# Kernel tuning notes

Hardware: AMD Instinct MI355X
Metric: run time of the kernel (lower is better)

The kernel has to match this reference:

```python
import jax, jax.numpy as jnp
import numpy as np

B, P, M, N, H = 2, 2048, 1024, 16, 64
NEG = 1e10


def setup_inputs() -> dict:
    key = jax.random.key(0)
    ks = jax.random.split(key, 8)
    std = 0.02
    return {
        "x": jax.random.normal(ks[0], (B, P, M), jnp.float32),
        "kernel_query": std * jax.random.normal(ks[1], (N, M, H), jnp.float32),
        "bias_query": jnp.zeros((N, H), jnp.float32),
        "kernel_key": std * jax.random.normal(ks[2], (N, M, H), jnp.float32),
        "bias_key": jnp.zeros((N, H), jnp.float32),
        "kernel_value": std * jax.random.normal(ks[3], (N, M, H), jnp.float32),
        "bias_value": jnp.zeros((N, H), jnp.float32),
        "kernel_out": std * jax.random.normal(ks[4], (N, H, M), jnp.float32),
        "bias_out": jnp.zeros((M,), jnp.float32),
    }


def reference(x, kernel_query, bias_query, kernel_key, bias_key,
              kernel_value, bias_value, kernel_out, bias_out):
    # per-head projections: [b,p,m] x [n,m,h] -> [b,p,n,h]
    q = jnp.einsum('bpm,nmh->bpnh', x, kernel_query) + bias_query
    k = jnp.einsum('bpm,nmh->bpnh', x, kernel_key) + bias_key
    v = jnp.einsum('bpm,nmh->bpnh', x, kernel_value) + bias_value

    # explicit score matrix [b,n,pq,pk]
    scores = jnp.einsum('bqnh,bknh->bnqk', q, k) / jnp.sqrt(jnp.float32(H))
    # faithful reproduction of original (inverted) mask: keep strictly-upper
    # triangle, subtract 1e10 elsewhere
    p = scores.shape[-1]
    mask = jnp.triu(jnp.ones((p, p), scores.dtype), k=1)  # [pq,pk]
    masked = scores * mask - NEG * (1.0 - mask)
    attn = jax.nn.softmax(masked, axis=-1)

    z = jnp.einsum('bknh,bnqk->bqnh', v, attn)
    return jnp.einsum('bqnh,nhm->bqm', z, kernel_out) + bias_out
```

## Files before the change

kernel.cpp:

```cpp
#include <hip/hip_runtime.h>

typedef __attribute__((ext_vector_type(8))) __bf16 bf16x8;
typedef __attribute__((ext_vector_type(4))) float  f32x4;
typedef unsigned short u16;
typedef unsigned int   u32;

__device__ __forceinline__ u16 f2b(float f) {
  u32 u = __builtin_bit_cast(u32, f);
  u32 r = (u + 0x7FFFu + ((u >> 16) & 1u)) >> 16;
  return (u16)r;
}

typedef __attribute__((address_space(3))) void lds_void;
typedef const __attribute__((address_space(1))) void gbl_void;

__device__ __forceinline__ void gload_lds16(const u16* g, u16* l) {
  __builtin_amdgcn_global_load_lds((gbl_void*)g, (lds_void*)l, 16, 0, 0);
}

#define QSCALE 0.18033688011112042f
#define MFIX   4.328085122666891f

__global__ __launch_bounds__(256) void prep_all(const float* __restrict__ x,
                                                const float* __restrict__ wq,
                                                const float* __restrict__ wk,
                                                const float* __restrict__ wv,
                                                const float* __restrict__ wo,
                                                u16* __restrict__ xb,
                                                u16* __restrict__ wbt,
                                                u16* __restrict__ wot) {
  int bid = blockIdx.x;
  int tid = threadIdx.x;
  if (bid < 4096) {
    int i = bid * 256 + tid;
    float4 v = ((const float4*)x)[i];
    ushort4 o;
    o.x = f2b(v.x); o.y = f2b(v.y); o.z = f2b(v.z); o.w = f2b(v.w);
    ((ushort4*)xb)[i] = o;
    return;
  }
  __shared__ float t[64][65];
  int sub = bid - 4096;
  const float* src; u16* dst; int sstride, dstride, r0, c0;
  if (sub < 768) {
    int proj = sub >> 8, rem = sub & 255;
    int ym = rem >> 4, xt = rem & 15;
    src = ((proj == 0) ? wq : (proj == 1) ? wk : wv) + (size_t)ym * 65536;
    dst = wbt + ((size_t)proj << 20) + (size_t)ym * 65536;
    sstride = 64; dstride = 1024; r0 = xt * 64; c0 = 0;
  } else {
    int s2 = sub - 768;
    src = wo; dst = wot;
    sstride = 1024; dstride = 1024;
    r0 = (s2 & 15) * 64; c0 = (s2 >> 4) * 64;
  }
  int rr = tid >> 2, q = tid & 3;
#pragma unroll
  for (int i = 0; i < 4; ++i) {
    float4 v = *(const float4*)&src[(size_t)(r0 + rr) * sstride + c0 + q * 16 + i * 4];
    t[rr][q * 16 + i * 4 + 0] = v.x;
    t[rr][q * 16 + i * 4 + 1] = v.y;
    t[rr][q * 16 + i * 4 + 2] = v.z;
    t[rr][q * 16 + i * 4 + 3] = v.w;
  }
  __syncthreads();
  int cc = rr;
#pragma unroll
  for (int i = 0; i < 4; ++i) {
    ushort4 o;
    o.x = f2b(t[q * 16 + i * 4 + 0][cc]);
    o.y = f2b(t[q * 16 + i * 4 + 1][cc]);
    o.z = f2b(t[q * 16 + i * 4 + 2][cc]);
    o.w = f2b(t[q * 16 + i * 4 + 3][cc]);
    *(ushort4*)&dst[(size_t)(c0 + cc) * dstride + r0 + q * 16 + i * 4] = o;
  }
}

__global__ __launch_bounds__(256) void gemm_qkv(const u16* __restrict__ xb,
                                                const u16* __restrict__ wbt,
                                                const float* __restrict__ bq,
                                                const float* __restrict__ bk,
                                                const float* __restrict__ bv,
                                                u16* __restrict__ qb,
                                                u16* __restrict__ kbf,
                                                u16* __restrict__ vtb) {
  __shared__ __align__(16) u16 As[128 * 32];
  __shared__ __align__(16) u16 Bs[64 * 32];
  f32x4 acc[4][2];
#pragma unroll
  for (int mi = 0; mi < 4; ++mi)
#pragma unroll
    for (int ni = 0; ni < 2; ++ni) acc[mi][ni] = (f32x4){0.f, 0.f, 0.f, 0.f};

  int bid = blockIdx.x;
  int rt = bid & 31, ct = bid >> 5;
  int R0 = rt * 128, C0 = ct * 64;

  int tid = threadIdx.x;
  int w = tid >> 6, l = tid & 63;
  int lr = l & 15, lg = l >> 4;
  int wr = w >> 1, wc = w & 1;

  for (int k0 = 0; k0 < 1024; k0 += 32) {
#pragma unroll
    for (int i = 0; i < 2; ++i) {
      int t = w * 2 + i;
      gload_lds16(xb + (size_t)(R0 + t * 16 + (l >> 2)) * 1024 + k0 + (l & 3) * 8, &As[t * 512]);
    }
    gload_lds16(wbt + (size_t)(C0 + w * 16 + (l >> 2)) * 1024 + k0 + (l & 3) * 8, &Bs[w * 512]);
    __syncthreads();
    bf16x8 af[4], bfr[2];
#pragma unroll
    for (int mi = 0; mi < 4; ++mi)
      af[mi] = *(const bf16x8*)&As[(wr * 64 + mi * 16 + lr) * 32 + lg * 8];
#pragma unroll
    for (int ni = 0; ni < 2; ++ni)
      bfr[ni] = *(const bf16x8*)&Bs[(wc * 32 + ni * 16 + lr) * 32 + lg * 8];
#pragma unroll
    for (int mi = 0; mi < 4; ++mi)
#pragma unroll
      for (int ni = 0; ni < 2; ++ni)
        acc[mi][ni] = __builtin_amdgcn_mfma_f32_16x16x32_bf16(af[mi], bfr[ni], acc[mi][ni], 0, 0, 0);
    __syncthreads();
  }

  int proj = C0 >> 10;
#pragma unroll
  for (int ni = 0; ni < 2; ++ni) {
    int col = C0 + wc * 32 + ni * 16 + lr;
    int within = col & 1023;
    int n = within >> 6, h = within & 63;
    const float* bias = (proj == 0) ? bq : (proj == 1 ? bk : bv);
    float badd = bias[within];
    float scl = (proj == 0) ? QSCALE : 1.0f;
#pragma unroll
    for (int mi = 0; mi < 4; ++mi) {
#pragma unroll
      for (int r = 0; r < 4; ++r) {
        int row = R0 + wr * 64 + mi * 16 + lg * 4 + r;
        int b = row >> 11, p = row & 2047;
        int bn = b * 16 + n;
        u16 u = f2b((acc[mi][ni][r] + badd) * scl);
        if (proj == 0)      qb [((size_t)bn * 2048 + p) * 64 + h] = u;
        else if (proj == 1) kbf[((size_t)bn * 2048 + p) * 64 + h] = u;
        else                vtb[(((size_t)bn * 32 + (p >> 6)) * 64 + h) * 64 + (p & 63)] = u;
      }
    }
  }
}

__global__ __launch_bounds__(256) void mean_v(const u16* __restrict__ vtb,
                                              u16* __restrict__ zb) {
  __shared__ float red[4][64];
  int bn = blockIdx.x;
  int w = threadIdx.x >> 6, h = threadIdx.x & 63;
  const u16* base = vtb + (size_t)bn * 131072 + (size_t)h * 64;
  float acc = 0.f;
  for (int pb = w; pb < 32; pb += 4) {
    const u16* r = base + (size_t)pb * 4096;
#pragma unroll
    for (int c = 0; c < 8; ++c) {
      bf16x8 v = *(const bf16x8*)(r + c * 8);
#pragma unroll
      for (int j = 0; j < 8; ++j) acc += (float)v[j];
    }
  }
  red[w][h] = acc;
  __syncthreads();
  if (w == 0) {
    float s = (red[0][h] + red[1][h] + red[2][h] + red[3][h]) * (1.0f / 2048.0f);
    int b = bn >> 4, n = bn & 15;
    zb[((size_t)(b * 2048 + 2047) * 16 + n) * 64 + h] = f2b(s);
  }
}

#define ATTN_STEP(BUFC, MASKED)                                                \
  {                                                                            \
    if (t + 1 < trips) {                                                       \
      gload_lds16(sk,       &Ks[BUFC ^ 1][w * 1024]);                          \
      gload_lds16(sk + 512, &Ks[BUFC ^ 1][w * 1024 + 512]);                    \
      gload_lds16(sv,       &Vs[BUFC ^ 1][w * 1024]);                          \
      gload_lds16(sv + 512, &Vs[BUFC ^ 1][w * 1024 + 512]);                    \
      sk += 4096; sv += 4096;                                                  \
      asm volatile("s_waitcnt vmcnt(4)" ::: "memory");                         \
    } else {                                                                   \
      asm volatile("s_waitcnt vmcnt(0)" ::: "memory");                         \
    }                                                                          \
    __builtin_amdgcn_s_barrier();                                              \
    asm volatile("" ::: "memory");                                             \
    f32x4 sacc[4];                                                             \
    __builtin_amdgcn_s_setprio(1);                                             \
    _Pragma("unroll") for (int nb = 0; nb < 4; ++nb) {                         \
      int row = nb * 16 + lr, sw = row & 7;                                    \
      bf16x8 kf0 = *(const bf16x8*)&Ks[BUFC][row * 64 + ((lg ^ sw) << 3)];     \
      bf16x8 kf1 = *(const bf16x8*)&Ks[BUFC][row * 64 + (((lg + 4) ^ sw) << 3)]; \
      f32x4 s = (f32x4){0.f, 0.f, 0.f, 0.f};                                   \
      s = __builtin_amdgcn_mfma_f32_16x16x32_bf16(qf0, kf0, s, 0, 0, 0);       \
      s = __builtin_amdgcn_mfma_f32_16x16x32_bf16(qf1, kf1, s, 0, 0, 0);       \
      sacc[nb] = s;                                                            \
    }                                                                          \
    __builtin_amdgcn_s_setprio(0);                                             \
    u16 pbv[4][4];                                                             \
    if (MASKED) {                                                              \
      _Pragma("unroll") for (int nb = 0; nb < 4; ++nb) {                       \
        int key = nb * 16 + lr;                                                \
        _Pragma("unroll") for (int r = 0; r < 4; ++r) {                        \
          int qrow = w * 16 + lg * 4 + r;                                      \
          float xv = (key > qrow) ? sacc[nb][r] : -1.0e10f;                    \
          float pe = __builtin_amdgcn_exp2f(xv - MFIX);                        \
          rsum[r] += pe;                                                       \
          pbv[nb][r] = __builtin_bit_cast(u16, (__bf16)pe);                    \
        }                                                                      \
      }                                                                        \
    } else {                                                                   \
      _Pragma("unroll") for (int nb = 0; nb < 4; ++nb)                         \
        _Pragma("unroll") for (int r = 0; r < 4; ++r) {                        \
          float pe = __builtin_amdgcn_exp2f(sacc[nb][r] - MFIX);               \
          rsum[r] += pe;                                                       \
          pbv[nb][r] = __builtin_bit_cast(u16, (__bf16)pe);                    \
        }                                                                      \
    }                                                                          \
    _Pragma("unroll") for (int nb = 0; nb < 4; ++nb)                           \
      _Pragma("unroll") for (int r = 0; r < 4; ++r) {                          \
        int prow = lg * 4 + r;                                                 \
        Plds[w][prow * 64 + ((((nb * 2) + (lr >> 3)) ^ (prow & 7)) << 3) + (lr & 7)] = pbv[nb][r]; \
      }                                                                        \
    asm volatile("s_waitcnt lgkmcnt(0)" ::: "memory");                         \
    __builtin_amdgcn_sched_barrier(0);                                         \
    bf16x8 pf0 = *(const bf16x8*)&Plds[w][lr * 64 + ((lg ^ (lr & 7)) << 3)];   \
    bf16x8 pf1 = *(const bf16x8*)&Plds[w][lr * 64 + (((4 + lg) ^ (lr & 7)) << 3)]; \
    __builtin_amdgcn_s_setprio(1);                                             \
    _Pragma("unroll") for (int hb = 0; hb < 4; ++hb) {                         \
      int row = hb * 16 + lr, sw = row & 7;                                    \
      bf16x8 vf0 = *(const bf16x8*)&Vs[BUFC][row * 64 + ((lg ^ sw) << 3)];     \
      bf16x8 vf1 = *(const bf16x8*)&Vs[BUFC][row * 64 + (((lg + 4) ^ sw) << 3)]; \
      oacc[hb] = __builtin_amdgcn_mfma_f32_16x16x32_bf16(pf0, vf0, oacc[hb], 0, 0, 0); \
      oacc[hb] = __builtin_amdgcn_mfma_f32_16x16x32_bf16(pf1, vf1, oacc[hb], 0, 0, 0); \
    }                                                                          \
    __builtin_amdgcn_s_setprio(0);                                             \
    asm volatile("" ::: "memory");                                             \
    __builtin_amdgcn_s_barrier();                                              \
    ++t;                                                                       \
  }

__global__ __launch_bounds__(256, 4) void attn_kern(const u16* __restrict__ qb,
                                                    const u16* __restrict__ kbf,
                                                    const u16* __restrict__ vtb,
                                                    u16* __restrict__ zb) {
  __shared__ __align__(16) u16 Ks[2][4096];
  __shared__ __align__(16) u16 Vs[2][4096];
  __shared__ __align__(16) u16 Plds[4][1024];

  int bid = blockIdx.x;
  int bn = bid & 31, c = bid >> 5;
  int trips = 32 - c;
  int tid = threadIdx.x;
  int w = tid >> 6, l = tid & 63;
  int lr = l & 15, lg = l >> 4;

  const u16* Q  = qb  + (size_t)bn * 131072;
  const u16* Kp = kbf + (size_t)bn * 131072;
  const u16* Vt = vtb + (size_t)bn * 131072;

  int row0 = w * 16 + (l >> 3), col8 = l & 7;
  int soff = row0 * 64 + ((col8 ^ (row0 & 7)) << 3);

  int q0w = c * 64 + w * 16;
  bf16x8 qf0 = *(const bf16x8*)&Q[(size_t)(q0w + lr) * 64 + lg * 8];
  bf16x8 qf1 = *(const bf16x8*)&Q[(size_t)(q0w + lr) * 64 + 32 + lg * 8];

  float rsum[4];
  f32x4 oacc[4];
#pragma unroll
  for (int r = 0; r < 4; ++r) rsum[r] = 0.0f;
#pragma unroll
  for (int hb = 0; hb < 4; ++hb) oacc[hb] = (f32x4){0.f, 0.f, 0.f, 0.f};

  const u16* sk = Kp + (size_t)c * 4096 + soff;
  const u16* sv = Vt + (size_t)c * 4096 + soff;
  gload_lds16(sk,       &Ks[0][w * 1024]);
  gload_lds16(sk + 512, &Ks[0][w * 1024 + 512]);
  gload_lds16(sv,       &Vs[0][w * 1024]);
  gload_lds16(sv + 512, &Vs[0][w * 1024 + 512]);
  sk += 4096; sv += 4096;

  int t = 0;
  ATTN_STEP(0, true)
  while (t + 1 < trips) {
    ATTN_STEP(1, false)
    ATTN_STEP(0, false)
  }
  if (t < trips) ATTN_STEP(1, false)

#pragma unroll
  for (int r = 0; r < 4; ++r) {
    float v = rsum[r];
    v += __shfl_xor(v, 1);
    v += __shfl_xor(v, 2);
    v += __shfl_xor(v, 4);
    v += __shfl_xor(v, 8);
    rsum[r] = 1.0f / v;
  }
  int b = bn >> 4, n = bn & 15;
#pragma unroll
  for (int hb = 0; hb < 4; ++hb) {
    int h = hb * 16 + lr;
#pragma unroll
    for (int r = 0; r < 4; ++r) {
      int qrow = q0w + lg * 4 + r;
      zb[((size_t)(b * 2048 + qrow) * 16 + n) * 64 + h] = f2b(oacc[hb][r] * rsum[r]);
    }
  }
}

__global__ __launch_bounds__(256) void gemm_out(const u16* __restrict__ zb,
                                                const u16* __restrict__ wot,
                                                const float* __restrict__ bo,
                                                float* __restrict__ out) {
  __shared__ __align__(16) u16 As[128 * 32];
  __shared__ __align__(16) u16 Bs[64 * 32];
  f32x4 acc[4][2];
#pragma unroll
  for (int mi = 0; mi < 4; ++mi)
#pragma unroll
    for (int ni = 0; ni < 2; ++ni) acc[mi][ni] = (f32x4){0.f, 0.f, 0.f, 0.f};

  int bid = (blockIdx.x & 7) * 64 + (blockIdx.x >> 3);
  int rt = bid >> 4, ct = bid & 15;
  int R0 = rt * 128, C0 = ct * 64;

  int tid = threadIdx.x;
  int w = tid >> 6, l = tid & 63;
  int lr = l & 15, lg = l >> 4;
  int wr = w >> 1, wc = w & 1;

  for (int k0 = 0; k0 < 1024; k0 += 32) {
#pragma unroll
    for (int i = 0; i < 2; ++i) {
      int t = w * 2 + i;
      gload_lds16(zb + (size_t)(R0 + t * 16 + (l >> 2)) * 1024 + k0 + (l & 3) * 8, &As[t * 512]);
    }
    gload_lds16(wot + (size_t)(C0 + w * 16 + (l >> 2)) * 1024 + k0 + (l & 3) * 8, &Bs[w * 512]);
    __syncthreads();
    bf16x8 af[4], bfr[2];
#pragma unroll
    for (int mi = 0; mi < 4; ++mi)
      af[mi] = *(const bf16x8*)&As[(wr * 64 + mi * 16 + lr) * 32 + lg * 8];
#pragma unroll
    for (int ni = 0; ni < 2; ++ni)
      bfr[ni] = *(const bf16x8*)&Bs[(wc * 32 + ni * 16 + lr) * 32 + lg * 8];
#pragma unroll
    for (int mi = 0; mi < 4; ++mi)
#pragma unroll
      for (int ni = 0; ni < 2; ++ni)
        acc[mi][ni] = __builtin_amdgcn_mfma_f32_16x16x32_bf16(af[mi], bfr[ni], acc[mi][ni], 0, 0, 0);
    __syncthreads();
  }

#pragma unroll
  for (int ni = 0; ni < 2; ++ni) {
    int col = C0 + wc * 32 + ni * 16 + lr;
    float badd = bo[col];
#pragma unroll
    for (int mi = 0; mi < 4; ++mi) {
#pragma unroll
      for (int r = 0; r < 4; ++r) {
        int row = R0 + wr * 64 + mi * 16 + lg * 4 + r;
        out[(size_t)row * 1024 + col] = acc[mi][ni][r] + badd;
      }
    }
  }
}

extern "C" void kernel_launch(void* const* d_in, const int* in_sizes, int n_in,
                              void* d_out, int out_size, void* d_ws, size_t ws_size,
                              hipStream_t stream) {
  const float* x  = (const float*)d_in[0];
  const float* wq = (const float*)d_in[1];
  const float* bq = (const float*)d_in[2];
  const float* wk = (const float*)d_in[3];
  const float* bk = (const float*)d_in[4];
  const float* wv = (const float*)d_in[5];
  const float* bv = (const float*)d_in[6];
  const float* wo = (const float*)d_in[7];
  const float* bo = (const float*)d_in[8];
  float* out = (float*)d_out;

  char* ws = (char*)d_ws;
  u16* xb  = (u16*)(ws + ((size_t)0 << 20));
  u16* wbt = (u16*)(ws + ((size_t)8 << 20));
  u16* wot = (u16*)(ws + ((size_t)14 << 20));
  u16* qb  = (u16*)(ws + ((size_t)16 << 20));
  u16* kbf = (u16*)(ws + ((size_t)24 << 20));
  u16* vtb = (u16*)(ws + ((size_t)32 << 20));
  u16* zb  = (u16*)(ws + ((size_t)40 << 20));

  prep_all<<<dim3(5120), dim3(256), 0, stream>>>(x, wq, wk, wv, wo, xb, wbt, wot);
  gemm_qkv<<<dim3(32 * 48), dim3(256), 0, stream>>>(xb, wbt, bq, bk, bv, qb, kbf, vtb);
  attn_kern<<<dim3(1024), dim3(256), 0, stream>>>(qb, kbf, vtb, zb);
  mean_v<<<dim3(32), dim3(256), 0, stream>>>(vtb, zb);
  gemm_out<<<dim3(32 * 16), dim3(256), 0, stream>>>(zb, wot, bo, out);
}
```

Measured before the change: 133.4 us.

## Rewrite QKV GEMM with 256x256 tiles and double-buffered async LDS loads

The QKV projection GEMM moves from 128x64 tiles with 256 threads and a single LDS buffer to 256x256 tiles with 512 threads, a 64-wide K step and two LDS buffers. The next K tile is prefetched with global_load_lds while MFMAs run, using explicit vmcnt waits and raw barriers, and s_setprio raises priority around the MFMA block. This targets low operand reuse and exposed load latency, but cuts the grid to 192 blocks on a GPU with many CUs, which risks leaving CUs idle. It also uses 128 KB of LDS per block, which may conflict with the occupancy of 2 requested in the launch bounds.

```diff
diff --git a/kernel.cpp b/kernel.cpp
--- a/kernel.cpp
+++ b/kernel.cpp
@@ -76,71 +76,92 @@
   }
 }
 
-__global__ __launch_bounds__(256) void gemm_qkv(const u16* __restrict__ xb,
-                                                const u16* __restrict__ wbt,
-                                                const float* __restrict__ bq,
-                                                const float* __restrict__ bk,
-                                                const float* __restrict__ bv,
-                                                u16* __restrict__ qb,
-                                                u16* __restrict__ kbf,
-                                                u16* __restrict__ vtb) {
-  __shared__ __align__(16) u16 As[128 * 32];
-  __shared__ __align__(16) u16 Bs[64 * 32];
-  f32x4 acc[4][2];
-#pragma unroll
-  for (int mi = 0; mi < 4; ++mi)
-#pragma unroll
-    for (int ni = 0; ni < 2; ++ni) acc[mi][ni] = (f32x4){0.f, 0.f, 0.f, 0.f};
+__global__ __launch_bounds__(512, 2) void gemm_qkv(const u16* __restrict__ xb,
+                                                   const u16* __restrict__ wbt,
+                                                   const float* __restrict__ bq,
+                                                   const float* __restrict__ bk,
+                                                   const float* __restrict__ bv,
+                                                   u16* __restrict__ qb,
+                                                   u16* __restrict__ kbf,
+                                                   u16* __restrict__ vtb) {
+  __shared__ __align__(16) u16 As[2][16384];
+  __shared__ __align__(16) u16 Bs[2][16384];
 
   int bid = blockIdx.x;
-  int rt = bid & 31, ct = bid >> 5;
-  int R0 = rt * 128, C0 = ct * 64;
+  int rt = bid & 15, ct = bid >> 4;
+  int R0 = rt * 256, C0 = ct * 256;
 
   int tid = threadIdx.x;
   int w = tid >> 6, l = tid & 63;
   int lr = l & 15, lg = l >> 4;
-  int wr = w >> 1, wc = w & 1;
-
-  for (int k0 = 0; k0 < 1024; k0 += 32) {
-#pragma unroll
-    for (int i = 0; i < 2; ++i) {
-      int t = w * 2 + i;
-      gload_lds16(xb + (size_t)(R0 + t * 16 + (l >> 2)) * 1024 + k0 + (l & 3) * 8, &As[t * 512]);
-    }
-    gload_lds16(wbt + (size_t)(C0 + w * 16 + (l >> 2)) * 1024 + k0 + (l & 3) * 8, &Bs[w * 512]);
-    __syncthreads();
-    bf16x8 af[4], bfr[2];
-#pragma unroll
-    for (int mi = 0; mi < 4; ++mi)
-      af[mi] = *(const bf16x8*)&As[(wr * 64 + mi * 16 + lr) * 32 + lg * 8];
-#pragma unroll
-    for (int ni = 0; ni < 2; ++ni)
-      bfr[ni] = *(const bf16x8*)&Bs[(wc * 32 + ni * 16 + lr) * 32 + lg * 8];
-#pragma unroll
-    for (int mi = 0; mi < 4; ++mi)
-#pragma unroll
-      for (int ni = 0; ni < 2; ++ni)
-        acc[mi][ni] = __builtin_amdgcn_mfma_f32_16x16x32_bf16(af[mi], bfr[ni], acc[mi][ni], 0, 0, 0);
-    __syncthreads();
+  int wm = w >> 2, wn = w & 3;
+  int rr = tid >> 3, cc8 = (tid & 7) * 8;
+
+  f32x4 acc[8][4];
+#pragma unroll
+  for (int m = 0; m < 8; ++m)
+#pragma unroll
+    for (int n = 0; n < 4; ++n) acc[m][n] = (f32x4){0.f, 0.f, 0.f, 0.f};
+
+  auto stage = [&](int kt, int buf) {
+#pragma unroll
+    for (int i = 0; i < 4; ++i)
+      gload_lds16(xb + (size_t)(R0 + i * 64 + rr) * 1024 + kt * 64 + cc8,
+                  &As[buf][i * 4096 + w * 512]);
+#pragma unroll
+    for (int i = 0; i < 4; ++i)
+      gload_lds16(wbt + (size_t)(C0 + i * 64 + rr) * 1024 + kt * 64 + cc8,
+                  &Bs[buf][i * 4096 + w * 512]);
+  };
+
+  stage(0, 0);
+  stage(1, 1);
+
+  for (int kt = 0; kt < 16; ++kt) {
+    int buf = kt & 1;
+    if (kt < 15) asm volatile("s_waitcnt vmcnt(8)" ::: "memory");
+    else         asm volatile("s_waitcnt vmcnt(0)" ::: "memory");
+    __builtin_amdgcn_s_barrier();
+    asm volatile("" ::: "memory");
+#pragma unroll
+    for (int kk = 0; kk < 2; ++kk) {
+      bf16x8 af[8], bfr[4];
+#pragma unroll
+      for (int m = 0; m < 8; ++m)
+        af[m] = *(const bf16x8*)&As[buf][(wm * 128 + m * 16 + lr) * 64 + kk * 32 + lg * 8];
+#pragma unroll
+      for (int n = 0; n < 4; ++n)
+        bfr[n] = *(const bf16x8*)&Bs[buf][(wn * 64 + n * 16 + lr) * 64 + kk * 32 + lg * 8];
+      __builtin_amdgcn_s_setprio(1);
+#pragma unroll
+      for (int m = 0; m < 8; ++m)
+#pragma unroll
+        for (int n = 0; n < 4; ++n)
+          acc[m][n] = __builtin_amdgcn_mfma_f32_16x16x32_bf16(af[m], bfr[n], acc[m][n], 0, 0, 0);
+      __builtin_amdgcn_s_setprio(0);
+    }
+    asm volatile("" ::: "memory");
+    __builtin_amdgcn_s_barrier();
+    if (kt + 2 < 16) stage(kt + 2, buf);
   }
 
   int proj = C0 >> 10;
 #pragma unroll
-  for (int ni = 0; ni < 2; ++ni) {
-    int col = C0 + wc * 32 + ni * 16 + lr;
+  for (int n = 0; n < 4; ++n) {
+    int col = C0 + wn * 64 + n * 16 + lr;
     int within = col & 1023;
-    int n = within >> 6, h = within & 63;
+    int hn = within >> 6, h = within & 63;
     const float* bias = (proj == 0) ? bq : (proj == 1 ? bk : bv);
     float badd = bias[within];
     float scl = (proj == 0) ? QSCALE : 1.0f;
 #pragma unroll
-    for (int mi = 0; mi < 4; ++mi) {
+    for (int m = 0; m < 8; ++m) {
 #pragma unroll
       for (int r = 0; r < 4; ++r) {
-        int row = R0 + wr * 64 + mi * 16 + lg * 4 + r;
+        int row = R0 + wm * 128 + m * 16 + lg * 4 + r;
         int b = row >> 11, p = row & 2047;
-        int bn = b * 16 + n;
-        u16 u = f2b((acc[mi][ni][r] + badd) * scl);
+        int bn = b * 16 + hn;
+        u16 u = f2b((acc[m][n][r] + badd) * scl);
         if (proj == 0)      qb [((size_t)bn * 2048 + p) * 64 + h] = u;
         else if (proj == 1) kbf[((size_t)bn * 2048 + p) * 64 + h] = u;
         else                vtb[(((size_t)bn * 32 + (p >> 6)) * 64 + h) * 64 + (p & 63)] = u;
@@ -396,7 +417,7 @@
   u16* zb  = (u16*)(ws + ((size_t)40 << 20));
 
   prep_all<<<dim3(5120), dim3(256), 0, stream>>>(x, wq, wk, wv, wo, xb, wbt, wot);
-  gemm_qkv<<<dim3(32 * 48), dim3(256), 0, stream>>>(xb, wbt, bq, bk, bv, qb, kbf, vtb);
+  gemm_qkv<<<dim3(16 * 12), dim3(512), 0, stream>>>(xb, wbt, bq, bk, bv, qb, kbf, vtb);
   attn_kern<<<dim3(1024), dim3(256), 0, stream>>>(qb, kbf, vtb, zb);
   mean_v<<<dim3(32), dim3(256), 0, stream>>>(vtb, zb);
   gemm_out<<<dim3(32 * 16), dim3(256), 0, stream>>>(zb, wot, bo, out);
```

Measured after the change: 150.4 us. 1.13x slower.
